# Kernel optimization log

Measured on AMD Instinct MI355X. Metric: run time of the kernel, lower is better.

## Reference

```python
import jax
import jax.numpy as jnp
from jax import lax
import numpy as np

INPUT_DIM = 784
HIDDEN_DIM = 1024
BATCH = 256
N_BINS = 10


def setup_inputs() -> dict:
    key = jax.random.key(0)
    k1, k2, k3, k4, k5 = jax.random.split(key, 5)
    # kaiming-normal-ish init scales (faithful in spirit; exact values irrelevant for math)
    W = jax.random.normal(k1, (HIDDEN_DIM, INPUT_DIM), dtype=jnp.float32) * np.sqrt(2.0 / INPUT_DIM)
    c = jnp.zeros((HIDDEN_DIM, 1), dtype=jnp.float32)
    V = jax.random.normal(k2, (INPUT_DIM, HIDDEN_DIM, N_BINS), dtype=jnp.float32) * np.sqrt(2.0 / N_BINS)
    b = jnp.zeros((INPUT_DIM, N_BINS), dtype=jnp.float32)
    x = jax.random.randint(k3, (BATCH, INPUT_DIM), 0, N_BINS, dtype=jnp.int32)
    return {"x": x, "W": W, "c": c, "V": V, "b": b}


def reference(x, W, c, V, b):
    # x: [B, D] int pixel bins; W: [H, D]; c: [H, 1]; V: [D, H, 10]; b: [D, 10]
    B = x.shape[0]
    xf = x.astype(jnp.float32)  # [B, D]
    a0 = jnp.broadcast_to(c[:, 0][None, :], (B, W.shape[0]))  # [B, H]

    def step(a, inp):
        Vi, bi, Wi, xi = inp  # Vi:[H,10], bi:[10], Wi:[H], xi:[B]
        h = jax.nn.sigmoid(a)                       # [B, H]
        p = jax.nn.softmax(h @ Vi + bi, axis=1)     # [B, 10]
        a = a + xi[:, None] * Wi[None, :]           # rank-1 update, matches x_i @ W[:,i].T
        return a, p

    _, p_seq = lax.scan(step, a0, (V, b, W.T, xf.T))  # p_seq: [D, B, 10]
    p_hat = jnp.transpose(p_seq, (1, 2, 0))            # [B, 10, D] == torch.stack(p_hat, dim=2)
    return p_hat
```

## Files before the change

kernel.cpp:

```cpp
#include <hip/hip_runtime.h>
#include <stdint.h>

#define D_DIM 784
#define H_DIM 1024
#define B_DIM 256
#define NBIN  10
#define G_CH  8
#define T_CH  98
#define BT    16
#define LOG2E 1.4426950408889634f

#define VPREP_BLKS D_DIM
#define WPREP_BLKS 208

typedef _Float16 half8_t  __attribute__((ext_vector_type(8)));
typedef __fp16   fp16x2_t __attribute__((ext_vector_type(2)));
typedef float    float4_t __attribute__((ext_vector_type(4)));

__global__ void k_prep(const float* __restrict__ W, const float* __restrict__ V,
                       _Float16* __restrict__ Wt2h, _Float16* __restrict__ VB) {
    __shared__ __align__(16) float smem[5120];
    int tid = threadIdx.x;
    int bx  = blockIdx.x;

    if (bx < VPREP_BLKS) {
        int i = bx;
        const float4* src = (const float4*)(V + (size_t)i * H_DIM * NBIN);
        uint4* dst = (uint4*)VB + (size_t)i * 2048;
        #pragma unroll
        for (int p = 0; p < 2; ++p) {
            if (p) __syncthreads();
            #pragma unroll
            for (int qv = 0; qv < 5; ++qv) {
                float4 v = src[p * 1280 + qv * 256 + tid];
                *((float4*)&smem[(qv * 256 + tid) * 4]) = v;
            }
            __syncthreads();
            #pragma unroll
            for (int qv = 0; qv < 4; ++qv) {
                int pair = p * 1024 + qv * 256 + tid;
                int kk = pair >> 6, ll = pair & 63;
                int n = ll & 15, hb = kk * 32 + ((ll >> 4) & 3) * 8;
                union { _Float16 hh[8]; uint4 u; } o;
                #pragma unroll
                for (int jj = 0; jj < 8; ++jj)
                    o.hh[jj] = (_Float16)((n < NBIN) ? smem[(hb + jj) * NBIN + n - p * 5120] : 0.0f);
                dst[pair] = o.u;
            }
        }
    } else {
        int qw = bx - VPREP_BLKS;
        int j0 = (qw % 13) * 64, h0 = (qw / 13) * 64;
        float (*t)[65] = (float(*)[65])smem;
        int tj = tid & 63, tr = tid >> 6;
        int j = j0 + tj;
        #pragma unroll
        for (int r = 0; r < 16; ++r) {
            int hh = tr * 16 + r;
            t[hh][tj] = (j < D_DIM) ? W[(size_t)(h0 + hh) * D_DIM + j] : 0.0f;
        }
        __syncthreads();
        #pragma unroll
        for (int r = 0; r < 16; ++r) {
            int jj = tr * 16 + r;
            int jo = j0 + jj;
            if (jo < D_DIM) Wt2h[(size_t)jo * H_DIM + h0 + tj] = (_Float16)(t[tj][jj] * LOG2E);
        }
    }
}

__global__ __launch_bounds__(256)
void k_pscan(const _Float16* __restrict__ Wt2h, const int* __restrict__ x,
             const float* __restrict__ c, _Float16* __restrict__ PA) {
    int b   = blockIdx.x;
    int hg  = blockIdx.y;
    int tid = threadIdx.x;
    int hcol = hg * 256 + tid;
    int h0   = hcol * 2;

    __shared__ float xs[D_DIM];
    if (tid < D_DIM / 4) {
        int4 xi = ((const int4*)(x + (size_t)b * D_DIM))[tid];
        *((float4*)&xs[tid * 4]) =
            make_float4((float)xi.x, (float)xi.y, (float)xi.z, (float)xi.w);
    }
    float acc0 = c[h0] * LOG2E, acc1 = c[h0 + 1] * LOG2E;
    __syncthreads();

    const uint* wp  = (const uint*)Wt2h;
    uint*       pau = (uint*)PA;

    uint wvA[8], wvB[8];
    auto ldrow = [&](int t, uint (&wv)[8]) {
        #pragma unroll
        for (int r = 0; r < 8; ++r)
            wv[r] = wp[(size_t)(t * 8 + r) * 512 + hcol];
    };
    auto emit = [&](int t) {
        union { _Float16 hh[2]; uint u; } uu;
        uu.hh[0] = (_Float16)acc0; uu.hh[1] = (_Float16)acc1;
        pau[((size_t)t * B_DIM + b) * 512 + hcol] = uu.u;
    };
    auto fmas = [&](int t, const uint (&wv)[8]) {
        #pragma unroll
        for (int r = 0; r < 8; ++r) {
            union { uint u; _Float16 hh[2]; } uu; uu.u = wv[r];
            float xf = xs[t * 8 + r];
            acc0 += xf * (float)uu.hh[0];
            acc1 += xf * (float)uu.hh[1];
        }
    };

    ldrow(0, wvA);
    for (int t = 0; t < T_CH; t += 2) {
        ldrow(t + 1, wvB);
        emit(t);
        fmas(t, wvA);
        if (t + 2 < T_CH) ldrow(t + 2, wvA);
        emit(t + 1);
        fmas(t + 1, wvB);
    }
}

__global__ __launch_bounds__(256, 4)
void k_main(const _Float16* __restrict__ VB, const _Float16* __restrict__ Wt2h,
            const _Float16* __restrict__ PA, const int* __restrict__ x,
            const float* __restrict__ bias, float* __restrict__ out) {
    int bt  = blockIdx.x;
    int tc  = blockIdx.y;
    int tid = threadIdx.x;
    int w   = tid >> 6;
    int l   = tid & 63;
    int bl  = l & 15;
    int kg  = l >> 4;
    int bg  = bt * BT + bl;
    int i0  = tc * G_CH;

    __shared__ __align__(16) _Float16 wlds[G_CH][H_DIM];
    __shared__ float red[4][64][18];
    __shared__ float bs[G_CH][16];

    {
        int ii = tid >> 4, n = tid & 15;
        if (ii < G_CH) bs[ii][n] = (n < NBIN) ? bias[(size_t)(i0 + ii) * NBIN + n] : 0.0f;
    }
    {
        #pragma unroll
        for (int r = 0; r < G_CH; ++r) {
            uint2 v = ((const uint2*)(Wt2h + (size_t)(i0 + r) * H_DIM))[tid];
            *((uint2*)&wlds[r][tid * 4]) = v;
        }
    }
    float xvf[G_CH];
    {
        const int4* xp = (const int4*)(x + (size_t)bg * D_DIM + i0);
        int4 x0 = xp[0], x1 = xp[1];
        xvf[0] = (float)x0.x; xvf[1] = (float)x0.y; xvf[2] = (float)x0.z; xvf[3] = (float)x0.w;
        xvf[4] = (float)x1.x; xvf[5] = (float)x1.y; xvf[6] = (float)x1.z; xvf[7] = (float)x1.w;
    }
    float a[8][8];
    {
        const _Float16* src = PA + ((size_t)tc * B_DIM + bg) * H_DIM + w * 256 + kg * 8;
        #pragma unroll
        for (int m = 0; m < 8; ++m) {
            half8_t av = *((const half8_t*)(src + m * 32));
            #pragma unroll
            for (int j = 0; j < 8; ++j) a[m][j] = (float)av[j];
        }
    }

    const uint4* vp = (const uint4*)VB + ((size_t)i0 * 32 + w * 8) * 64 + l;
    uint4 vbuf[3];
    vbuf[0] = vp[0];
    vbuf[1] = vp[64];
    float4_t acc = {0.f, 0.f, 0.f, 0.f};

    auto step = [&](int mm) {
        const int ii = mm >> 3, m = mm & 7;
        if (mm + 2 < 64) {
            const int nn = mm + 2;
            vbuf[nn % 3] = vp[((nn >> 3) * 32 + (nn & 7)) * 64];
        }
        union { half8_t h8; uint u32[4]; } af;
        #pragma unroll
        for (int p = 0; p < 4; ++p) {
            float s0 = __builtin_amdgcn_rcpf(1.0f + __builtin_amdgcn_exp2f(-a[m][2 * p]));
            float s1 = __builtin_amdgcn_rcpf(1.0f + __builtin_amdgcn_exp2f(-a[m][2 * p + 1]));
            union { fp16x2_t v; uint u; } cv;
            cv.v = __builtin_amdgcn_cvt_pkrtz(s0, s1);
            af.u32[p] = cv.u;
        }
        union { half8_t h8; uint4 u; } bf;
        bf.u = vbuf[mm % 3];
        acc = __builtin_amdgcn_mfma_f32_16x16x32_f16(af.h8, bf.h8, acc, 0, 0, 0);
        half8_t wh = *((const half8_t*)&wlds[ii][w * 256 + kg * 8 + m * 32]);
        float xf = xvf[ii];
        a[m][0] += xf * (float)wh[0]; a[m][1] += xf * (float)wh[1];
        a[m][2] += xf * (float)wh[2]; a[m][3] += xf * (float)wh[3];
        a[m][4] += xf * (float)wh[4]; a[m][5] += xf * (float)wh[5];
        a[m][6] += xf * (float)wh[6]; a[m][7] += xf * (float)wh[7];
        if (m == 7) {
            int s = (ii & 3) * 4;
            red[w][l][s + 0] = acc[0]; red[w][l][s + 1] = acc[1];
            red[w][l][s + 2] = acc[2]; red[w][l][s + 3] = acc[3];
            acc = (float4_t){0.f, 0.f, 0.f, 0.f};
        }
    };

    auto softmax_store = [&](int half) {
        float p4[4];
        #pragma unroll
        for (int q = 0; q < 4; ++q) {
            int ii = half * 4 + q;
            float tot = red[0][l][q * 4 + w] + red[1][l][q * 4 + w]
                      + red[2][l][q * 4 + w] + red[3][l][q * 4 + w];
            float v = (bl < NBIN) ? tot + bs[ii][bl] : -3.0e38f;
            float vm = v;
            vm = fmaxf(vm, __shfl_xor(vm, 1));
            vm = fmaxf(vm, __shfl_xor(vm, 2));
            vm = fmaxf(vm, __shfl_xor(vm, 4));
            vm = fmaxf(vm, __shfl_xor(vm, 8));
            float e = __builtin_amdgcn_exp2f((v - vm) * LOG2E);
            float ss = e;
            ss += __shfl_xor(ss, 1); ss += __shfl_xor(ss, 2);
            ss += __shfl_xor(ss, 4); ss += __shfl_xor(ss, 8);
            p4[q] = e * __builtin_amdgcn_rcpf(ss);
        }
        if (bl < NBIN) {
            int b = bt * BT + kg * 4 + w;
            size_t base = ((size_t)b * NBIN + bl) * D_DIM + i0 + half * 4;
            float4 v = make_float4(p4[0], p4[1], p4[2], p4[3]);
            *((float4*)(out + base)) = v;
        }
    };

    __syncthreads();
    #pragma unroll
    for (int mm = 0; mm < 32; ++mm) step(mm);
    __syncthreads();
    softmax_store(0);
    __syncthreads();
    #pragma unroll
    for (int mm = 32; mm < 64; ++mm) step(mm);
    __syncthreads();
    softmax_store(1);
}

extern "C" void kernel_launch(void* const* d_in, const int* in_sizes, int n_in,
                              void* d_out, int out_size, void* d_ws, size_t ws_size,
                              hipStream_t stream) {
    const int*   x    = (const int*)d_in[0];
    const float* W    = (const float*)d_in[1];
    const float* c    = (const float*)d_in[2];
    const float* V    = (const float*)d_in[3];
    const float* bias = (const float*)d_in[4];
    float* out = (float*)d_out;

    char* ws = (char*)d_ws;
    size_t off = 0;
    _Float16* Wt2h = (_Float16*)(ws + off);
    off += (size_t)D_DIM * H_DIM * sizeof(_Float16);
    off = (off + 255) & ~(size_t)255;
    _Float16* VB = (_Float16*)(ws + off);
    off += (size_t)D_DIM * 32 * 64 * 8 * sizeof(_Float16);
    off = (off + 255) & ~(size_t)255;
    _Float16* PA = (_Float16*)(ws + off);

    k_prep<<<dim3(VPREP_BLKS + WPREP_BLKS), 256, 0, stream>>>(W, V, Wt2h, VB);
    k_pscan<<<dim3(B_DIM, 2), 256, 0, stream>>>(Wt2h, x, c, PA);
    k_main<<<dim3(B_DIM / BT, T_CH), 256, 0, stream>>>(VB, Wt2h, PA, x, bias, out);
}
```

Before: 191.9 us.

## Double chunk length, stream W from global, double-buffer reductions, swizzle block order

Chunk size doubles from 8 to 16 columns, which halves the number of prefix checkpoints k_pscan writes and k_main reads. k_main now streams W rows straight from global into a register double buffer instead of staging them in LDS. It double-buffers the reduction array so each quarter needs one barrier instead of two. A 1D grid with a swizzled block index spreads tiles across XCDs, and launch bounds drop to 3 blocks per SIMD to allow more registers. The gain is less PA traffic and fewer syncs, at the cost of longer serial work per block and possibly lower occupancy.

```diff
diff --git a/kernel.cpp b/kernel.cpp
--- a/kernel.cpp
+++ b/kernel.cpp
@@ -5,8 +5,8 @@
 #define H_DIM 1024
 #define B_DIM 256
 #define NBIN  10
-#define G_CH  8
-#define T_CH  98
+#define G_CH  16
+#define T_CH  49
 #define BT    16
 #define LOG2E 1.4426950408889634f
 
@@ -90,44 +90,45 @@
     const uint* wp  = (const uint*)Wt2h;
     uint*       pau = (uint*)PA;
 
-    uint wvA[8], wvB[8];
-    auto ldrow = [&](int t, uint (&wv)[8]) {
-        #pragma unroll
-        for (int r = 0; r < 8; ++r)
-            wv[r] = wp[(size_t)(t * 8 + r) * 512 + hcol];
+    uint wvA[16], wvB[16];
+    auto ldrow = [&](int t, uint (&wv)[16]) {
+        #pragma unroll
+        for (int r = 0; r < 16; ++r)
+            wv[r] = wp[(size_t)(t * 16 + r) * 512 + hcol];
     };
     auto emit = [&](int t) {
         union { _Float16 hh[2]; uint u; } uu;
         uu.hh[0] = (_Float16)acc0; uu.hh[1] = (_Float16)acc1;
         pau[((size_t)t * B_DIM + b) * 512 + hcol] = uu.u;
     };
-    auto fmas = [&](int t, const uint (&wv)[8]) {
-        #pragma unroll
-        for (int r = 0; r < 8; ++r) {
+    auto fmas = [&](int t, const uint (&wv)[16]) {
+        #pragma unroll
+        for (int r = 0; r < 16; ++r) {
             union { uint u; _Float16 hh[2]; } uu; uu.u = wv[r];
-            float xf = xs[t * 8 + r];
+            float xf = xs[t * 16 + r];
             acc0 += xf * (float)uu.hh[0];
             acc1 += xf * (float)uu.hh[1];
         }
     };
 
     ldrow(0, wvA);
-    for (int t = 0; t < T_CH; t += 2) {
+    for (int t = 0; t < T_CH - 1; t += 2) {
         ldrow(t + 1, wvB);
-        emit(t);
-        fmas(t, wvA);
-        if (t + 2 < T_CH) ldrow(t + 2, wvA);
-        emit(t + 1);
-        fmas(t + 1, wvB);
-    }
-}
-
-__global__ __launch_bounds__(256, 4)
+        emit(t);     fmas(t, wvA);
+        ldrow(t + 2, wvA);
+        emit(t + 1); fmas(t + 1, wvB);
+    }
+    emit(T_CH - 1);
+}
+
+__global__ __launch_bounds__(256, 3)
 void k_main(const _Float16* __restrict__ VB, const _Float16* __restrict__ Wt2h,
             const _Float16* __restrict__ PA, const int* __restrict__ x,
             const float* __restrict__ bias, float* __restrict__ out) {
-    int bt  = blockIdx.x;
-    int tc  = blockIdx.y;
+    int bid = blockIdx.x;
+    int lb  = (bid & 7) * 98 + (bid >> 3);
+    int tc  = lb >> 4;
+    int bt  = lb & 15;
     int tid = threadIdx.x;
     int w   = tid >> 6;
     int l   = tid & 63;
@@ -136,28 +137,14 @@
     int bg  = bt * BT + bl;
     int i0  = tc * G_CH;
 
-    __shared__ __align__(16) _Float16 wlds[G_CH][H_DIM];
-    __shared__ float red[4][64][18];
+    __shared__ float red[2][4][64][17];
     __shared__ float bs[G_CH][16];
 
     {
         int ii = tid >> 4, n = tid & 15;
-        if (ii < G_CH) bs[ii][n] = (n < NBIN) ? bias[(size_t)(i0 + ii) * NBIN + n] : 0.0f;
-    }
-    {
-        #pragma unroll
-        for (int r = 0; r < G_CH; ++r) {
-            uint2 v = ((const uint2*)(Wt2h + (size_t)(i0 + r) * H_DIM))[tid];
-            *((uint2*)&wlds[r][tid * 4]) = v;
-        }
-    }
-    float xvf[G_CH];
-    {
-        const int4* xp = (const int4*)(x + (size_t)bg * D_DIM + i0);
-        int4 x0 = xp[0], x1 = xp[1];
-        xvf[0] = (float)x0.x; xvf[1] = (float)x0.y; xvf[2] = (float)x0.z; xvf[3] = (float)x0.w;
-        xvf[4] = (float)x1.x; xvf[5] = (float)x1.y; xvf[6] = (float)x1.z; xvf[7] = (float)x1.w;
-    }
+        bs[ii][n] = (n < NBIN) ? bias[(size_t)(i0 + ii) * NBIN + n] : 0.0f;
+    }
+
     float a[8][8];
     {
         const _Float16* src = PA + ((size_t)tc * B_DIM + bg) * H_DIM + w * 256 + kg * 8;
@@ -169,52 +156,30 @@
         }
     }
 
+    const int4* xp = (const int4*)(x + (size_t)bg * D_DIM + i0);
+
     const uint4* vp = (const uint4*)VB + ((size_t)i0 * 32 + w * 8) * 64 + l;
-    uint4 vbuf[3];
+    uint4 vbuf[4];
     vbuf[0] = vp[0];
     vbuf[1] = vp[64];
+    const uint4* vpr = vp + 128;
+
+    const _Float16* whp = Wt2h + (size_t)i0 * H_DIM + w * 256 + kg * 8;
+    half8_t whbuf[2];
+    whbuf[0] = *((const half8_t*)whp);
+    whbuf[1] = *((const half8_t*)(whp + 32));
+    const _Float16* whr = whp + 64;
+
     float4_t acc = {0.f, 0.f, 0.f, 0.f};
 
-    auto step = [&](int mm) {
-        const int ii = mm >> 3, m = mm & 7;
-        if (mm + 2 < 64) {
-            const int nn = mm + 2;
-            vbuf[nn % 3] = vp[((nn >> 3) * 32 + (nn & 7)) * 64];
-        }
-        union { half8_t h8; uint u32[4]; } af;
-        #pragma unroll
-        for (int p = 0; p < 4; ++p) {
-            float s0 = __builtin_amdgcn_rcpf(1.0f + __builtin_amdgcn_exp2f(-a[m][2 * p]));
-            float s1 = __builtin_amdgcn_rcpf(1.0f + __builtin_amdgcn_exp2f(-a[m][2 * p + 1]));
-            union { fp16x2_t v; uint u; } cv;
-            cv.v = __builtin_amdgcn_cvt_pkrtz(s0, s1);
-            af.u32[p] = cv.u;
-        }
-        union { half8_t h8; uint4 u; } bf;
-        bf.u = vbuf[mm % 3];
-        acc = __builtin_amdgcn_mfma_f32_16x16x32_f16(af.h8, bf.h8, acc, 0, 0, 0);
-        half8_t wh = *((const half8_t*)&wlds[ii][w * 256 + kg * 8 + m * 32]);
-        float xf = xvf[ii];
-        a[m][0] += xf * (float)wh[0]; a[m][1] += xf * (float)wh[1];
-        a[m][2] += xf * (float)wh[2]; a[m][3] += xf * (float)wh[3];
-        a[m][4] += xf * (float)wh[4]; a[m][5] += xf * (float)wh[5];
-        a[m][6] += xf * (float)wh[6]; a[m][7] += xf * (float)wh[7];
-        if (m == 7) {
-            int s = (ii & 3) * 4;
-            red[w][l][s + 0] = acc[0]; red[w][l][s + 1] = acc[1];
-            red[w][l][s + 2] = acc[2]; red[w][l][s + 3] = acc[3];
-            acc = (float4_t){0.f, 0.f, 0.f, 0.f};
-        }
-    };
-
-    auto softmax_store = [&](int half) {
+    auto softmax_store = [&](int q) {
+        const int buf = q & 1;
         float p4[4];
         #pragma unroll
-        for (int q = 0; q < 4; ++q) {
-            int ii = half * 4 + q;
-            float tot = red[0][l][q * 4 + w] + red[1][l][q * 4 + w]
-                      + red[2][l][q * 4 + w] + red[3][l][q * 4 + w];
-            float v = (bl < NBIN) ? tot + bs[ii][bl] : -3.0e38f;
+        for (int qq = 0; qq < 4; ++qq) {
+            float tot = red[buf][0][l][qq * 4 + w] + red[buf][1][l][qq * 4 + w]
+                      + red[buf][2][l][qq * 4 + w] + red[buf][3][l][qq * 4 + w];
+            float v = (bl < NBIN) ? tot + bs[q * 4 + qq][bl] : -3.0e38f;
             float vm = v;
             vm = fmaxf(vm, __shfl_xor(vm, 1));
             vm = fmaxf(vm, __shfl_xor(vm, 2));
@@ -224,26 +189,56 @@
             float ss = e;
             ss += __shfl_xor(ss, 1); ss += __shfl_xor(ss, 2);
             ss += __shfl_xor(ss, 4); ss += __shfl_xor(ss, 8);
-            p4[q] = e * __builtin_amdgcn_rcpf(ss);
+            p4[qq] = e * __builtin_amdgcn_rcpf(ss);
         }
         if (bl < NBIN) {
             int b = bt * BT + kg * 4 + w;
-            size_t base = ((size_t)b * NBIN + bl) * D_DIM + i0 + half * 4;
-            float4 v = make_float4(p4[0], p4[1], p4[2], p4[3]);
-            *((float4*)(out + base)) = v;
-        }
-    };
-
-    __syncthreads();
-    #pragma unroll
-    for (int mm = 0; mm < 32; ++mm) step(mm);
-    __syncthreads();
-    softmax_store(0);
-    __syncthreads();
-    #pragma unroll
-    for (int mm = 32; mm < 64; ++mm) step(mm);
-    __syncthreads();
-    softmax_store(1);
+            size_t base = ((size_t)b * NBIN + bl) * D_DIM + i0 + q * 4;
+            *((float4*)(out + base)) = make_float4(p4[0], p4[1], p4[2], p4[3]);
+        }
+    };
+
+    for (int q = 0; q < 4; ++q) {
+        int4 xi = xp[q];
+        float xq0 = (float)xi.x, xq1 = (float)xi.y, xq2 = (float)xi.z, xq3 = (float)xi.w;
+        #pragma unroll
+        for (int s = 0; s < 32; ++s) {
+            const int iis = s >> 3;
+            const int m   = s & 7;
+            const int nn  = q * 32 + s + 2;
+            half8_t wh = whbuf[s & 1];
+            if (nn < 128) {
+                vbuf[(s + 2) & 3] = *vpr;
+                whbuf[s & 1] = *((const half8_t*)whr);
+                vpr += (((s + 3) & 7) == 0) ? 1600 : 64;
+                whr += (((s + 3) & 7) == 0) ? 800  : 32;
+            }
+            union { half8_t h8; uint u32[4]; } af;
+            #pragma unroll
+            for (int p = 0; p < 4; ++p) {
+                float s0 = __builtin_amdgcn_rcpf(1.0f + __builtin_amdgcn_exp2f(-a[m][2 * p]));
+                float s1 = __builtin_amdgcn_rcpf(1.0f + __builtin_amdgcn_exp2f(-a[m][2 * p + 1]));
+                union { fp16x2_t v; uint u; } cv;
+                cv.v = __builtin_amdgcn_cvt_pkrtz(s0, s1);
+                af.u32[p] = cv.u;
+            }
+            union { half8_t h8; uint4 u; } bf;
+            bf.u = vbuf[s & 3];
+            acc = __builtin_amdgcn_mfma_f32_16x16x32_f16(af.h8, bf.h8, acc, 0, 0, 0);
+            float xf = (iis == 0) ? xq0 : (iis == 1) ? xq1 : (iis == 2) ? xq2 : xq3;
+            a[m][0] += xf * (float)wh[0]; a[m][1] += xf * (float)wh[1];
+            a[m][2] += xf * (float)wh[2]; a[m][3] += xf * (float)wh[3];
+            a[m][4] += xf * (float)wh[4]; a[m][5] += xf * (float)wh[5];
+            a[m][6] += xf * (float)wh[6]; a[m][7] += xf * (float)wh[7];
+            if (m == 7) {
+                float* rp = &red[q & 1][w][l][iis * 4];
+                rp[0] = acc[0]; rp[1] = acc[1]; rp[2] = acc[2]; rp[3] = acc[3];
+                acc = (float4_t){0.f, 0.f, 0.f, 0.f};
+            }
+        }
+        __syncthreads();
+        softmax_store(q);
+    }
 }
 
 extern "C" void kernel_launch(void* const* d_in, const int* in_sizes, int n_in,
@@ -268,5 +263,5 @@
 
     k_prep<<<dim3(VPREP_BLKS + WPREP_BLKS), 256, 0, stream>>>(W, V, Wt2h, VB);
     k_pscan<<<dim3(B_DIM, 2), 256, 0, stream>>>(Wt2h, x, c, PA);
-    k_main<<<dim3(B_DIM / BT, T_CH), 256, 0, stream>>>(VB, Wt2h, PA, x, bias, out);
-}
+    k_main<<<dim3(D_DIM), 256, 0, stream>>>(VB, Wt2h, PA, x, bias, out);
+}
```

After: 204.4 us. +6.5%, slower.
